# Optimization experiments

Hardware: AMD Instinct MI355X
Metric: run time of the kernel (lower is better)

Reference implementation:

```python
import jax, jax.numpy as jnp
import numpy as np

D_MODEL = 1024
N_HEADS = 16
HEAD_DIM = D_MODEL // N_HEADS


def setup_inputs() -> dict:
    key = jax.random.key(0)
    ks = jax.random.split(key, 5)
    B, T = 4, 2048
    x = jax.random.normal(ks[0], (B, T, D_MODEL), dtype=jnp.float32)
    s_in = 1.0 / np.sqrt(D_MODEL)
    W_qkv = jax.random.normal(ks[1], (D_MODEL, 3 * D_MODEL), dtype=jnp.float32) * s_in
    b_qkv = jnp.zeros((3 * D_MODEL,), dtype=jnp.float32)
    W_proj = jax.random.normal(ks[2], (D_MODEL, D_MODEL), dtype=jnp.float32) * s_in
    b_proj = jnp.zeros((D_MODEL,), dtype=jnp.float32)
    return {"x": x, "W_qkv": W_qkv, "b_qkv": b_qkv, "W_proj": W_proj, "b_proj": b_proj}


def reference(x, W_qkv, b_qkv, W_proj, b_proj):
    B, T, C = x.shape
    qkv = x @ W_qkv + b_qkv                       # [B, T, 3C]
    q, k, v = jnp.split(qkv, 3, axis=-1)
    def heads(t):  # [B, T, C] -> [B, H, T, Dh]
        return t.reshape(B, T, N_HEADS, HEAD_DIM).transpose(0, 2, 1, 3)
    q, k, v = heads(q), heads(k), heads(v)
    scale = 1.0 / np.sqrt(HEAD_DIM)
    att = jnp.einsum('bhqd,bhkd->bhqk', q, k) * scale   # [B, H, T, T]
    causal = jnp.tril(jnp.ones((T, T), dtype=bool))
    att = jnp.where(causal, att, -jnp.inf)
    att = jax.nn.softmax(att, axis=-1)
    out = jnp.einsum('bhqk,bhkd->bhqd', att, v)          # [B, H, T, Dh]
    out = out.transpose(0, 2, 1, 3).reshape(B, T, C)
    return out @ W_proj + b_proj
```

## Files before the change

### kernel.cpp

```cpp
#include <hip/hip_runtime.h>
#include <hip/hip_bf16.h>

#define NH 16
#define HD 64
#define T_SEQ 2048
#define DM 1024

typedef __attribute__((ext_vector_type(8))) short short8;
typedef __attribute__((ext_vector_type(4))) short sh4;
typedef __attribute__((ext_vector_type(4))) float f32x4;
typedef unsigned short ushort;

static __device__ __forceinline__ float bf2f(short u) {
    unsigned int x = ((unsigned int)(unsigned short)u) << 16;
    union { unsigned int i; float f; } c; c.i = x; return c.f;
}
static __device__ __forceinline__ ushort f2bf(float f) {
    union { float f; unsigned int u; } c; c.f = f;
    unsigned int r = (c.u + 0x7fffu + ((c.u >> 16) & 1u)) >> 16;
    return (ushort)r;
}

static __device__ __forceinline__ void gload16(const ushort* g, ushort* l) {
    __builtin_amdgcn_global_load_lds(
        (const __attribute__((address_space(1))) void*)(const void*)g,
        (__attribute__((address_space(3))) void*)(void*)l, 16, 0, 0);
}

__global__ __launch_bounds__(256) void conv_bf16(const float* __restrict__ src,
                                                 ushort* __restrict__ dst) {
    int i = blockIdx.x * 256 + threadIdx.x;
    const float* s = src + (size_t)i * 8;
    float4 a = *(const float4*)(s);
    float4 b = *(const float4*)(s + 4);
    short8 o;
    o[0] = f2bf(a.x); o[1] = f2bf(a.y); o[2] = f2bf(a.z); o[3] = f2bf(a.w);
    o[4] = f2bf(b.x); o[5] = f2bf(b.y); o[6] = f2bf(b.z); o[7] = f2bf(b.w);
    *(short8*)(dst + (size_t)i * 8) = o;
}

__global__ __launch_bounds__(256) void transpose_w(const float* __restrict__ W,
                                                   ushort* __restrict__ Wt, int N) {
    __shared__ float Ts[64][65];
    const int n0 = blockIdx.x * 64, k0 = blockIdx.y * 64;
    const int tid = threadIdx.x;
    const int cg = tid & 15, r4 = tid >> 4;
    #pragma unroll
    for (int i = 0; i < 4; ++i) {
        int r = r4 + i * 16;
        float4 v = *(const float4*)(W + (size_t)(k0 + r) * N + n0 + cg * 4);
        Ts[r][cg * 4 + 0] = v.x; Ts[r][cg * 4 + 1] = v.y;
        Ts[r][cg * 4 + 2] = v.z; Ts[r][cg * 4 + 3] = v.w;
    }
    __syncthreads();
    #pragma unroll
    for (int i = 0; i < 4; ++i) {
        int r = r4 + i * 16;
        sh4 o;
        o[0] = (short)f2bf(Ts[cg * 4 + 0][r]);
        o[1] = (short)f2bf(Ts[cg * 4 + 1][r]);
        o[2] = (short)f2bf(Ts[cg * 4 + 2][r]);
        o[3] = (short)f2bf(Ts[cg * 4 + 3][r]);
        *(sh4*)(Wt + (size_t)(n0 + r) * DM + k0 + cg * 4) = o;
    }
}

static __device__ __forceinline__ void gemm_core(
    const ushort* __restrict__ A, const ushort* __restrict__ Bt,
    ushort* __restrict__ As, ushort* __restrict__ Bs,
    int m0, int n0, f32x4 acc[4][4])
{
    const int tid = threadIdx.x;
    const int wid = tid >> 6, lane = tid & 63;
    const int lr = lane & 15, g = lane >> 4;
    const int wm = wid >> 1, wn = wid & 1;

    const int lrow = lane >> 3;
    const int lslot = lane & 7;

    for (int kt = 0; kt < 16; ++kt) {
        const int k0 = kt * 64;
        #pragma unroll
        for (int i = 0; i < 4; ++i) {
            const int row = wid * 32 + i * 8 + lrow;
            const int gcol = ((lslot ^ (row & 7)) * 8);
            const int ldsoff = (wid * 32 + i * 8) * 64;
            gload16(A  + (size_t)(m0 + row) * DM + k0 + gcol, As + ldsoff);
            gload16(Bt + (size_t)(n0 + row) * DM + k0 + gcol, Bs + ldsoff);
        }
        __syncthreads();
        #pragma unroll
        for (int ks = 0; ks < 2; ++ks) {
            short8 af[4], bfr[4];
            #pragma unroll
            for (int mi = 0; mi < 4; ++mi) {
                int row = wm * 64 + mi * 16 + lr;
                af[mi] = *(const short8*)(As + row * 64 + (((ks * 4 + g) ^ (row & 7)) * 8));
            }
            #pragma unroll
            for (int ni = 0; ni < 4; ++ni) {
                int row = wn * 64 + ni * 16 + lr;
                bfr[ni] = *(const short8*)(Bs + row * 64 + (((ks * 4 + g) ^ (row & 7)) * 8));
            }
            #pragma unroll
            for (int mi = 0; mi < 4; ++mi)
                #pragma unroll
                for (int ni = 0; ni < 4; ++ni)
                    acc[mi][ni] = __builtin_amdgcn_mfma_f32_16x16x32_bf16(af[mi], bfr[ni], acc[mi][ni], 0, 0, 0);
        }
        __syncthreads();
    }
}

__global__ __launch_bounds__(256) void qkv_mfma(
    const ushort* __restrict__ Xb, const ushort* __restrict__ Wqt,
    const float* __restrict__ bias,
    ushort* __restrict__ Qb, ushort* __restrict__ Kb, ushort* __restrict__ Vt)
{
    __shared__ __align__(16) ushort smem[16384];
    ushort* As = smem; ushort* Bs = smem + 8192;
    const int m0 = blockIdx.y * 128;
    const int n0 = blockIdx.x * 128;
    f32x4 acc[4][4] = {};
    gemm_core(Xb, Wqt, As, Bs, m0, n0, acc);

    const int tid = threadIdx.x;
    const int wid = tid >> 6, lane = tid & 63;
    const int lr = lane & 15, g = lane >> 4;
    const int wm = wid >> 1, wn = wid & 1;
    const int which = n0 >> 10;
    const int bq = m0 >> 11;

    if (which < 2) {
        ushort* dst = which ? Kb : Qb;
        const float sc = which ? 1.0f : 0.125f * 1.44269504f;
        #pragma unroll
        for (int ni = 0; ni < 4; ++ni) {
            int nn = n0 + wn * 64 + ni * 16 + lr;
            const float bv = bias[nn];
            const int hh = (nn & 1023) >> 6, dd = nn & 63;
            const size_t hb = ((size_t)(bq * NH + hh)) * T_SEQ;
            #pragma unroll
            for (int mi = 0; mi < 4; ++mi)
                #pragma unroll
                for (int r = 0; r < 4; ++r) {
                    int t = (m0 + wm * 64 + mi * 16 + g * 4 + r) & 2047;
                    dst[(hb + t) * HD + dd] = f2bf((acc[mi][ni][r] + bv) * sc);
                }
        }
    } else {
        __syncthreads();
        ushort* Ct = smem;
        #pragma unroll
        for (int ni = 0; ni < 4; ++ni) {
            int lcol = wn * 64 + ni * 16 + lr;
            const float bv = bias[n0 + lcol];
            #pragma unroll
            for (int mi = 0; mi < 4; ++mi)
                #pragma unroll
                for (int r = 0; r < 4; ++r)
                    Ct[(wm * 64 + mi * 16 + g * 4 + r) * 128 + lcol] = f2bf(acc[mi][ni][r] + bv);
        }
        __syncthreads();
        const int dloc = tid >> 1, th = (tid & 1) * 64;
        const int nn = (n0 & 1023) + dloc;
        ushort* dst = Vt + ((size_t)(bq * 1024 + nn)) * T_SEQ + (m0 & 2047) + th;
        #pragma unroll
        for (int e8 = 0; e8 < 8; ++e8) {
            short8 v;
            #pragma unroll
            for (int u = 0; u < 8; ++u) v[u] = (short)Ct[(th + e8 * 8 + u) * 128 + dloc];
            *(short8*)(dst + e8 * 8) = v;
        }
    }
}

__global__ __launch_bounds__(256) void proj_mfma(
    const ushort* __restrict__ AO, const ushort* __restrict__ Wpt,
    const float* __restrict__ bias, float* __restrict__ Y)
{
    __shared__ __align__(16) ushort smem[16384];
    const int m0 = blockIdx.y * 128;
    const int n0 = blockIdx.x * 128;
    f32x4 acc[4][4] = {};
    gemm_core(AO, Wpt, smem, smem + 8192, m0, n0, acc);

    const int tid = threadIdx.x;
    const int wid = tid >> 6, lane = tid & 63;
    const int lr = lane & 15, g = lane >> 4;
    const int wm = wid >> 1, wn = wid & 1;
    #pragma unroll
    for (int ni = 0; ni < 4; ++ni) {
        int nn = n0 + wn * 64 + ni * 16 + lr;
        const float bv = bias[nn];
        #pragma unroll
        for (int mi = 0; mi < 4; ++mi)
            #pragma unroll
            for (int r = 0; r < 4; ++r) {
                int m = m0 + wm * 64 + mi * 16 + g * 4 + r;
                Y[(size_t)m * DM + nn] = acc[mi][ni][r] + bv;
            }
    }
}

__global__ __launch_bounds__(256) void attn_mfma(
    const ushort* __restrict__ Qb,
    const ushort* __restrict__ Kb,
    const ushort* __restrict__ Vt,
    ushort* __restrict__ AO)
{
    __shared__ __align__(16) ushort Ks[2][4096];
    __shared__ __align__(16) ushort Vs[2][4096];

    const int bh = blockIdx.x;
    const int j = 15 - blockIdx.y;
    const int tid = threadIdx.x;
    const int wid = tid >> 6;
    const int lane = tid & 63;
    const int lr = lane & 15;
    const int g = lane >> 4;

    const ushort* Kg = Kb + (size_t)bh * T_SEQ * HD;
    const ushort* Vg = Vt + (size_t)bh * HD * T_SEQ;

    const int srow = tid >> 3;
    const int sco = (tid & 7) * 8;
    const int ssw = sco ^ ((srow & 7) << 3);
    const int sdst0 = srow * 64 + ssw;
    const int sdst1 = (srow + 32) * 64 + ssw;

    const int srcA = ((lane >> 4) & 1) * 32 + lr;
    const int srcB = srcA + 16;
    const bool selhi = (lane >> 5) != 0;

    const int b = bh >> 4, h = bh & 15;
    ushort* AOg = AO + (size_t)b * T_SEQ * DM + h * HD;

    const int q0 = j * 128;
    const int qlo = q0 + wid * 32;
    const int ntiles = 2 * j + 2;

    short8 qb[2][2];
    {
        const ushort* Qg = Qb + ((size_t)bh * T_SEQ + qlo) * HD;
        #pragma unroll
        for (int qi = 0; qi < 2; ++qi)
            #pragma unroll
            for (int ks = 0; ks < 2; ++ks)
                qb[qi][ks] = *(const short8*)(Qg + (size_t)(qi * 16 + lr) * HD + ks * 32 + g * 8);
    }

    f32x4 po[2][4] = {};
    float lp[2] = {0.f, 0.f};

    short8 rk0, rk1, rv0, rv1;
    rk0 = *(const short8*)(Kg + (size_t)srow * HD + sco);
    rk1 = *(const short8*)(Kg + (size_t)(srow + 32) * HD + sco);
    rv0 = *(const short8*)(Vg + (size_t)srow * T_SEQ + sco);
    rv1 = *(const short8*)(Vg + (size_t)(srow + 32) * T_SEQ + sco);
    *(short8*)(&Ks[0][sdst0]) = rk0;  *(short8*)(&Ks[0][sdst1]) = rk1;
    *(short8*)(&Vs[0][sdst0]) = rv0;  *(short8*)(&Vs[0][sdst1]) = rv1;
    {
        const int nk0 = 64;
        rk0 = *(const short8*)(Kg + (size_t)(nk0 + srow) * HD + sco);
        rk1 = *(const short8*)(Kg + (size_t)(nk0 + srow + 32) * HD + sco);
        rv0 = *(const short8*)(Vg + (size_t)srow * T_SEQ + nk0 + sco);
        rv1 = *(const short8*)(Vg + (size_t)(srow + 32) * T_SEQ + nk0 + sco);
    }
    __syncthreads();

    for (int tt = 0; tt < ntiles; ++tt) {
        const int k0 = tt * 64;
        const int cur = tt & 1;
        if (tt + 1 < ntiles) {
            const int nxt = cur ^ 1;
            *(short8*)(&Ks[nxt][sdst0]) = rk0;  *(short8*)(&Ks[nxt][sdst1]) = rk1;
            *(short8*)(&Vs[nxt][sdst0]) = rv0;  *(short8*)(&Vs[nxt][sdst1]) = rv1;
            if (tt + 2 < ntiles) {
                const int nk0 = (tt + 2) * 64;
                rk0 = *(const short8*)(Kg + (size_t)(nk0 + srow) * HD + sco);
                rk1 = *(const short8*)(Kg + (size_t)(nk0 + srow + 32) * HD + sco);
                rv0 = *(const short8*)(Vg + (size_t)srow * T_SEQ + nk0 + sco);
                rv1 = *(const short8*)(Vg + (size_t)(srow + 32) * T_SEQ + nk0 + sco);
            }
        }

        if (k0 <= qlo + 31) {
            const ushort* ksb = Ks[cur];
            const ushort* vsb = Vs[cur];

            short8 vf[2][4];
            #pragma unroll
            for (int ks = 0; ks < 2; ++ks)
                #pragma unroll
                for (int di = 0; di < 4; ++di) {
                    int vrow = di * 16 + lr;
                    vf[ks][di] = *(const short8*)(&vsb[vrow * 64 + ((ks * 32 + g * 8) ^ ((vrow & 7) << 3))]);
                }

            f32x4 sp[2][4] = {};
            __builtin_amdgcn_s_setprio(1);
            #pragma unroll
            for (int ks = 0; ks < 2; ++ks) {
                #pragma unroll
                for (int ki = 0; ki < 4; ++ki) {
                    int krow = ki * 16 + lr;
                    short8 kf = *(const short8*)(&ksb[krow * 64 + ((ks * 32 + g * 8) ^ ((krow & 7) << 3))]);
                    sp[0][ki] = __builtin_amdgcn_mfma_f32_16x16x32_bf16(kf, qb[0][ks], sp[0][ki], 0, 0, 0);
                    sp[1][ki] = __builtin_amdgcn_mfma_f32_16x16x32_bf16(kf, qb[1][ks], sp[1][ki], 0, 0, 0);
                }
            }
            __builtin_amdgcn_s_setprio(0);

            const bool needmask = (k0 + 63 > qlo);

            #pragma unroll
            for (int qi = 0; qi < 2; ++qi) {
                if (needmask) {
                    const int lim = qlo + qi * 16 + lr - k0 - 4 * g;
                    #pragma unroll
                    for (int ki = 0; ki < 4; ++ki)
                        #pragma unroll
                        for (int r = 0; r < 4; ++r)
                            sp[qi][ki][r] = (ki * 16 + r <= lim) ? sp[qi][ki][r] : -INFINITY;
                }
                float rs = 0.f;
                #pragma unroll
                for (int ki = 0; ki < 4; ++ki)
                    #pragma unroll
                    for (int r = 0; r < 4; ++r) {
                        float p;
                        asm("v_exp_f32 %0, %1" : "=v"(p) : "v"(sp[qi][ki][r]));
                        sp[qi][ki][r] = p;
                        rs += p;
                    }
                lp[qi] += rs;

                unsigned int u[4][2];
                #pragma unroll
                for (int ki = 0; ki < 4; ++ki) {
                    asm("v_cvt_pk_bf16_f32 %0, %1, %2"
                        : "=v"(u[ki][0]) : "v"(sp[qi][ki][0]), "v"(sp[qi][ki][1]));
                    asm("v_cvt_pk_bf16_f32 %0, %1, %2"
                        : "=v"(u[ki][1]) : "v"(sp[qi][ki][2]), "v"(sp[qi][ki][3]));
                }
                #pragma unroll
                for (int ks = 0; ks < 2; ++ks) {
                    const int a0 = (int)u[2 * ks][0],     a1 = (int)u[2 * ks][1];
                    const int b0 = (int)u[2 * ks + 1][0], b1 = (int)u[2 * ks + 1][1];
                    const int lo0 = __shfl(a0, srcA), lo1 = __shfl(a1, srcA);
                    const int lo2 = __shfl(a0, srcB), lo3 = __shfl(a1, srcB);
                    const int hi0 = __shfl(b0, srcA), hi1 = __shfl(b1, srcA);
                    const int hi2 = __shfl(b0, srcB), hi3 = __shfl(b1, srcB);
                    union { int w[4]; short8 s8; } pb;
                    pb.w[0] = selhi ? hi0 : lo0;
                    pb.w[1] = selhi ? hi1 : lo1;
                    pb.w[2] = selhi ? hi2 : lo2;
                    pb.w[3] = selhi ? hi3 : lo3;
                    __builtin_amdgcn_s_setprio(1);
                    #pragma unroll
                    for (int di = 0; di < 4; ++di)
                        po[qi][di] = __builtin_amdgcn_mfma_f32_16x16x32_bf16(vf[ks][di], pb.s8, po[qi][di], 0, 0, 0);
                    __builtin_amdgcn_s_setprio(0);
                }
            }
        }
        __syncthreads();
    }

    #pragma unroll
    for (int qi = 0; qi < 2; ++qi) {
        float l = lp[qi];
        l += __shfl_xor(l, 16);
        l += __shfl_xor(l, 32);
        const float inv = 1.f / l;
        const int q = qlo + qi * 16 + lr;
        #pragma unroll
        for (int di = 0; di < 4; ++di) {
            unsigned int w0, w1;
            float f0 = po[qi][di][0] * inv, f1 = po[qi][di][1] * inv;
            float f2 = po[qi][di][2] * inv, f3 = po[qi][di][3] * inv;
            asm("v_cvt_pk_bf16_f32 %0, %1, %2" : "=v"(w0) : "v"(f0), "v"(f1));
            asm("v_cvt_pk_bf16_f32 %0, %1, %2" : "=v"(w1) : "v"(f2), "v"(f3));
            uint2 wv; wv.x = w0; wv.y = w1;
            *(uint2*)(AOg + (size_t)q * DM + di * 16 + g * 4) = wv;
        }
    }
}

extern "C" void kernel_launch(void* const* d_in, const int* in_sizes, int n_in,
                              void* d_out, int out_size, void* d_ws, size_t ws_size,
                              hipStream_t stream) {
    const float* x      = (const float*)d_in[0];
    const float* W_qkv  = (const float*)d_in[1];
    const float* b_qkv  = (const float*)d_in[2];
    const float* W_proj = (const float*)d_in[3];
    const float* b_proj = (const float*)d_in[4];
    float* out = (float*)d_out;

    const size_t perbuf = (size_t)4 * NH * T_SEQ * HD;
    ushort* Qb  = (ushort*)d_ws;
    ushort* Kb  = Qb + perbuf;
    ushort* Vt  = Kb + perbuf;
    ushort* AO  = Vt + perbuf;
    ushort* Wqt = AO;
    ushort* Wpt = Qb;
    ushort* Xb  = (ushort*)d_out;

    hipLaunchKernelGGL(conv_bf16, dim3(4096), dim3(256), 0, stream, x, Xb);
    hipLaunchKernelGGL(transpose_w, dim3(48, 16), dim3(256), 0, stream, W_qkv, Wqt, 3 * DM);
    hipLaunchKernelGGL(qkv_mfma, dim3(24, 64), dim3(256), 0, stream,
                       Xb, Wqt, b_qkv, Qb, Kb, Vt);
    hipLaunchKernelGGL(attn_mfma, dim3(64, 16), dim3(256), 0, stream,
                       Qb, Kb, Vt, AO);
    hipLaunchKernelGGL(transpose_w, dim3(16, 16), dim3(256), 0, stream, W_proj, Wpt, DM);
    hipLaunchKernelGGL(proj_mfma, dim3(8, 64), dim3(256), 0, stream,
                       AO, Wpt, b_proj, out);
}
```

Measured before the change: 184.7 us.

## Double-buffer GEMM LDS loads and switch attention to 32x32x16 MFMA

```diff
diff --git a/kernel.cpp b/kernel.cpp
--- a/kernel.cpp
+++ b/kernel.cpp
@@ -9,12 +9,9 @@
 typedef __attribute__((ext_vector_type(8))) short short8;
 typedef __attribute__((ext_vector_type(4))) short sh4;
 typedef __attribute__((ext_vector_type(4))) float f32x4;
+typedef __attribute__((ext_vector_type(16))) float f32x16;
 typedef unsigned short ushort;
 
-static __device__ __forceinline__ float bf2f(short u) {
-    unsigned int x = ((unsigned int)(unsigned short)u) << 16;
-    union { unsigned int i; float f; } c; c.i = x; return c.f;
-}
 static __device__ __forceinline__ ushort f2bf(float f) {
     union { float f; unsigned int u; } c; c.f = f;
     unsigned int r = (c.u + 0x7fffu + ((c.u >> 16) & 1u)) >> 16;
@@ -67,28 +64,41 @@
 
 static __device__ __forceinline__ void gemm_core(
     const ushort* __restrict__ A, const ushort* __restrict__ Bt,
-    ushort* __restrict__ As, ushort* __restrict__ Bs,
-    int m0, int n0, f32x4 acc[4][4])
+    ushort* __restrict__ smem, int m0, int n0, f32x4 acc[4][4])
 {
     const int tid = threadIdx.x;
     const int wid = tid >> 6, lane = tid & 63;
     const int lr = lane & 15, g = lane >> 4;
     const int wm = wid >> 1, wn = wid & 1;
-
-    const int lrow = lane >> 3;
-    const int lslot = lane & 7;
-
-    for (int kt = 0; kt < 16; ++kt) {
-        const int k0 = kt * 64;
+    const int lrow = lane >> 3, lslot = lane & 7;
+
+    auto stage = [&](int b, int kt) {
+        ushort* As = smem + b * 16384;
+        ushort* Bs = As + 8192;
         #pragma unroll
         for (int i = 0; i < 4; ++i) {
             const int row = wid * 32 + i * 8 + lrow;
-            const int gcol = ((lslot ^ (row & 7)) * 8);
+            const int gcol = (lslot ^ (row & 7)) * 8;
             const int ldsoff = (wid * 32 + i * 8) * 64;
-            gload16(A  + (size_t)(m0 + row) * DM + k0 + gcol, As + ldsoff);
-            gload16(Bt + (size_t)(n0 + row) * DM + k0 + gcol, Bs + ldsoff);
-        }
-        __syncthreads();
+            gload16(A  + (size_t)(m0 + row) * DM + kt * 64 + gcol, As + ldsoff);
+            gload16(Bt + (size_t)(n0 + row) * DM + kt * 64 + gcol, Bs + ldsoff);
+        }
+    };
+
+    stage(0, 0);
+    #pragma unroll 1
+    for (int kt = 0; kt < 16; ++kt) {
+        const int cur = kt & 1;
+        if (kt < 15) {
+            stage(cur ^ 1, kt + 1);
+            asm volatile("s_waitcnt vmcnt(8)" ::: "memory");
+        } else {
+            asm volatile("s_waitcnt vmcnt(0)" ::: "memory");
+        }
+        __builtin_amdgcn_s_barrier();
+        __builtin_amdgcn_sched_barrier(0);
+        const ushort* As = smem + cur * 16384;
+        const ushort* Bs = As + 8192;
         #pragma unroll
         for (int ks = 0; ks < 2; ++ks) {
             short8 af[4], bfr[4];
@@ -108,7 +118,8 @@
                 for (int ni = 0; ni < 4; ++ni)
                     acc[mi][ni] = __builtin_amdgcn_mfma_f32_16x16x32_bf16(af[mi], bfr[ni], acc[mi][ni], 0, 0, 0);
         }
-        __syncthreads();
+        __builtin_amdgcn_sched_barrier(0);
+        __builtin_amdgcn_s_barrier();
     }
 }
 
@@ -117,12 +128,11 @@
     const float* __restrict__ bias,
     ushort* __restrict__ Qb, ushort* __restrict__ Kb, ushort* __restrict__ Vt)
 {
-    __shared__ __align__(16) ushort smem[16384];
-    ushort* As = smem; ushort* Bs = smem + 8192;
+    __shared__ __align__(16) ushort smem[32768];
     const int m0 = blockIdx.y * 128;
     const int n0 = blockIdx.x * 128;
     f32x4 acc[4][4] = {};
-    gemm_core(Xb, Wqt, As, Bs, m0, n0, acc);
+    gemm_core(Xb, Wqt, smem, m0, n0, acc);
 
     const int tid = threadIdx.x;
     const int wid = tid >> 6, lane = tid & 63;
@@ -179,11 +189,11 @@
     const ushort* __restrict__ AO, const ushort* __restrict__ Wpt,
     const float* __restrict__ bias, float* __restrict__ Y)
 {
-    __shared__ __align__(16) ushort smem[16384];
+    __shared__ __align__(16) ushort smem[32768];
     const int m0 = blockIdx.y * 128;
     const int n0 = blockIdx.x * 128;
     f32x4 acc[4][4] = {};
-    gemm_core(AO, Wpt, smem, smem + 8192, m0, n0, acc);
+    gemm_core(AO, Wpt, smem, m0, n0, acc);
 
     const int tid = threadIdx.x;
     const int wid = tid >> 6, lane = tid & 63;
@@ -217,8 +227,8 @@
     const int tid = threadIdx.x;
     const int wid = tid >> 6;
     const int lane = tid & 63;
-    const int lr = lane & 15;
-    const int g = lane >> 4;
+    const int ql = lane & 31;
+    const int hi = lane >> 5;
 
     const ushort* Kg = Kb + (size_t)bh * T_SEQ * HD;
     const ushort* Vg = Vt + (size_t)bh * HD * T_SEQ;
@@ -229,10 +239,6 @@
     const int sdst0 = srow * 64 + ssw;
     const int sdst1 = (srow + 32) * 64 + ssw;
 
-    const int srcA = ((lane >> 4) & 1) * 32 + lr;
-    const int srcB = srcA + 16;
-    const bool selhi = (lane >> 5) != 0;
-
     const int b = bh >> 4, h = bh & 15;
     ushort* AOg = AO + (size_t)b * T_SEQ * DM + h * HD;
 
@@ -240,18 +246,16 @@
     const int qlo = q0 + wid * 32;
     const int ntiles = 2 * j + 2;
 
-    short8 qb[2][2];
+    short8 qb[4];
     {
         const ushort* Qg = Qb + ((size_t)bh * T_SEQ + qlo) * HD;
         #pragma unroll
-        for (int qi = 0; qi < 2; ++qi)
-            #pragma unroll
-            for (int ks = 0; ks < 2; ++ks)
-                qb[qi][ks] = *(const short8*)(Qg + (size_t)(qi * 16 + lr) * HD + ks * 32 + g * 8);
-    }
-
-    f32x4 po[2][4] = {};
-    float lp[2] = {0.f, 0.f};
+        for (int ds = 0; ds < 4; ++ds)
+            qb[ds] = *(const short8*)(Qg + (size_t)ql * HD + ds * 16 + hi * 8);
+    }
+
+    f32x16 po[2] = {};
+    float lp = 0.f;
 
     short8 rk0, rk1, rv0, rv1;
     rk0 = *(const short8*)(Kg + (size_t)srow * HD + sco);
@@ -291,76 +295,74 @@
 
             short8 vf[2][4];
             #pragma unroll
-            for (int ks = 0; ks < 2; ++ks)
-                #pragma unroll
-                for (int di = 0; di < 4; ++di) {
-                    int vrow = di * 16 + lr;
-                    vf[ks][di] = *(const short8*)(&vsb[vrow * 64 + ((ks * 32 + g * 8) ^ ((vrow & 7) << 3))]);
-                }
-
-            f32x4 sp[2][4] = {};
+            for (int db = 0; db < 2; ++db)
+                #pragma unroll
+                for (int sl = 0; sl < 4; ++sl) {
+                    int row = db * 32 + ql;
+                    int slot = (sl * 2 + hi) ^ (row & 7);
+                    vf[db][sl] = *(const short8*)(&vsb[row * 64 + slot * 8]);
+                }
+
+            f32x16 sp[2] = {};
             __builtin_amdgcn_s_setprio(1);
             #pragma unroll
-            for (int ks = 0; ks < 2; ++ks) {
-                #pragma unroll
-                for (int ki = 0; ki < 4; ++ki) {
-                    int krow = ki * 16 + lr;
-                    short8 kf = *(const short8*)(&ksb[krow * 64 + ((ks * 32 + g * 8) ^ ((krow & 7) << 3))]);
-                    sp[0][ki] = __builtin_amdgcn_mfma_f32_16x16x32_bf16(kf, qb[0][ks], sp[0][ki], 0, 0, 0);
-                    sp[1][ki] = __builtin_amdgcn_mfma_f32_16x16x32_bf16(kf, qb[1][ks], sp[1][ki], 0, 0, 0);
+            for (int kb = 0; kb < 2; ++kb) {
+                #pragma unroll
+                for (int ds = 0; ds < 4; ++ds) {
+                    int row = kb * 32 + ql;
+                    int slot = (ds * 2 + hi) ^ (row & 7);
+                    short8 kf = *(const short8*)(&ksb[row * 64 + slot * 8]);
+                    sp[kb] = __builtin_amdgcn_mfma_f32_32x32x16_bf16(kf, qb[ds], sp[kb], 0, 0, 0);
                 }
             }
             __builtin_amdgcn_s_setprio(0);
 
-            const bool needmask = (k0 + 63 > qlo);
-
-            #pragma unroll
-            for (int qi = 0; qi < 2; ++qi) {
-                if (needmask) {
-                    const int lim = qlo + qi * 16 + lr - k0 - 4 * g;
+            if (k0 + 63 > qlo) {
+                #pragma unroll
+                for (int kb = 0; kb < 2; ++kb) {
+                    const int lim = qlo + ql - k0 - kb * 32 - 4 * hi;
                     #pragma unroll
-                    for (int ki = 0; ki < 4; ++ki)
-                        #pragma unroll
-                        for (int r = 0; r < 4; ++r)
-                            sp[qi][ki][r] = (ki * 16 + r <= lim) ? sp[qi][ki][r] : -INFINITY;
-                }
-                float rs = 0.f;
-                #pragma unroll
-                for (int ki = 0; ki < 4; ++ki)
-                    #pragma unroll
-                    for (int r = 0; r < 4; ++r) {
-                        float p;
-                        asm("v_exp_f32 %0, %1" : "=v"(p) : "v"(sp[qi][ki][r]));
-                        sp[qi][ki][r] = p;
-                        rs += p;
+                    for (int r = 0; r < 16; ++r) {
+                        const int c = (r & 3) + 8 * (r >> 2);
+                        sp[kb][r] = (c <= lim) ? sp[kb][r] : -INFINITY;
                     }
-                lp[qi] += rs;
-
-                unsigned int u[4][2];
-                #pragma unroll
-                for (int ki = 0; ki < 4; ++ki) {
-                    asm("v_cvt_pk_bf16_f32 %0, %1, %2"
-                        : "=v"(u[ki][0]) : "v"(sp[qi][ki][0]), "v"(sp[qi][ki][1]));
-                    asm("v_cvt_pk_bf16_f32 %0, %1, %2"
-                        : "=v"(u[ki][1]) : "v"(sp[qi][ki][2]), "v"(sp[qi][ki][3]));
-                }
-                #pragma unroll
-                for (int ks = 0; ks < 2; ++ks) {
-                    const int a0 = (int)u[2 * ks][0],     a1 = (int)u[2 * ks][1];
-                    const int b0 = (int)u[2 * ks + 1][0], b1 = (int)u[2 * ks + 1][1];
-                    const int lo0 = __shfl(a0, srcA), lo1 = __shfl(a1, srcA);
-                    const int lo2 = __shfl(a0, srcB), lo3 = __shfl(a1, srcB);
-                    const int hi0 = __shfl(b0, srcA), hi1 = __shfl(b1, srcA);
-                    const int hi2 = __shfl(b0, srcB), hi3 = __shfl(b1, srcB);
-                    union { int w[4]; short8 s8; } pb;
-                    pb.w[0] = selhi ? hi0 : lo0;
-                    pb.w[1] = selhi ? hi1 : lo1;
-                    pb.w[2] = selhi ? hi2 : lo2;
-                    pb.w[3] = selhi ? hi3 : lo3;
+                }
+            }
+
+            float rs = 0.f;
+            #pragma unroll
+            for (int kb = 0; kb < 2; ++kb)
+                #pragma unroll
+                for (int r = 0; r < 16; ++r) {
+                    float p;
+                    asm("v_exp_f32 %0, %1" : "=v"(p) : "v"(sp[kb][r]));
+                    sp[kb][r] = p;
+                    rs += p;
+                }
+            lp += rs;
+
+            #pragma unroll
+            for (int kb = 0; kb < 2; ++kb) {
+                #pragma unroll
+                for (int ks16 = 0; ks16 < 2; ++ks16) {
+                    unsigned int x0, x1, y0, y1;
+                    const int rb0 = ks16 * 2, rb1 = ks16 * 2 + 1;
+                    asm("v_cvt_pk_bf16_f32 %0, %1, %2" : "=v"(x0)
+                        : "v"(sp[kb][4 * rb0 + 0]), "v"(sp[kb][4 * rb0 + 1]));
+                    asm("v_cvt_pk_bf16_f32 %0, %1, %2" : "=v"(x1)
+                        : "v"(sp[kb][4 * rb0 + 2]), "v"(sp[kb][4 * rb0 + 3]));
+                    asm("v_cvt_pk_bf16_f32 %0, %1, %2" : "=v"(y0)
+                        : "v"(sp[kb][4 * rb1 + 0]), "v"(sp[kb][4 * rb1 + 1]));
+                    asm("v_cvt_pk_bf16_f32 %0, %1, %2" : "=v"(y1)
+                        : "v"(sp[kb][4 * rb1 + 2]), "v"(sp[kb][4 * rb1 + 3]));
+                    asm("v_permlane32_swap_b32 %0, %1" : "+v"(x0), "+v"(y0));
+                    asm("v_permlane32_swap_b32 %0, %1" : "+v"(x1), "+v"(y1));
+                    union { unsigned int w[4]; short8 s8; } pb;
+                    pb.w[0] = x0; pb.w[1] = x1; pb.w[2] = y0; pb.w[3] = y1;
+                    const int sl = kb * 2 + ks16;
                     __builtin_amdgcn_s_setprio(1);
-                    #pragma unroll
-                    for (int di = 0; di < 4; ++di)
-                        po[qi][di] = __builtin_amdgcn_mfma_f32_16x16x32_bf16(vf[ks][di], pb.s8, po[qi][di], 0, 0, 0);
+                    po[0] = __builtin_amdgcn_mfma_f32_32x32x16_bf16(vf[0][sl], pb.s8, po[0], 0, 0, 0);
+                    po[1] = __builtin_amdgcn_mfma_f32_32x32x16_bf16(vf[1][sl], pb.s8, po[1], 0, 0, 0);
                     __builtin_amdgcn_s_setprio(0);
                 }
             }
@@ -368,22 +370,20 @@
         __syncthreads();
     }
 
+    lp += __shfl_xor(lp, 32);
+    const float inv = 1.f / lp;
+    const int q = qlo + ql;
     #pragma unroll
-    for (int qi = 0; qi < 2; ++qi) {
-        float l = lp[qi];
-        l += __shfl_xor(l, 16);
-        l += __shfl_xor(l, 32);
-        const float inv = 1.f / l;
-        const int q = qlo + qi * 16 + lr;
-        #pragma unroll
-        for (int di = 0; di < 4; ++di) {
+    for (int db = 0; db < 2; ++db) {
+        #pragma unroll
+        for (int rb = 0; rb < 4; ++rb) {
             unsigned int w0, w1;
-            float f0 = po[qi][di][0] * inv, f1 = po[qi][di][1] * inv;
-            float f2 = po[qi][di][2] * inv, f3 = po[qi][di][3] * inv;
+            float f0 = po[db][4 * rb + 0] * inv, f1 = po[db][4 * rb + 1] * inv;
+            float f2 = po[db][4 * rb + 2] * inv, f3 = po[db][4 * rb + 3] * inv;
             asm("v_cvt_pk_bf16_f32 %0, %1, %2" : "=v"(w0) : "v"(f0), "v"(f1));
             asm("v_cvt_pk_bf16_f32 %0, %1, %2" : "=v"(w1) : "v"(f2), "v"(f3));
             uint2 wv; wv.x = w0; wv.y = w1;
-            *(uint2*)(AOg + (size_t)q * DM + di * 16 + g * 4) = wv;
+            *(uint2*)(AOg + (size_t)q * DM + db * 32 + 8 * rb + 4 * hi) = wv;
         }
     }
 }
```

After: 159.5 us. 1.16x faster.
